# Optimization experiments

Measured on AMD Instinct MI355X. Metric: run time of the kernel, lower is better.

Reference implementation:

```python
import jax, jax.numpy as jnp
import numpy as np

N = 100000
E = 1600000
U_DIM = 8
H_DIM = 64
MLP_H = 32
LRELU_SLOPE = 0.01  # torch LeakyReLU default


def _linear_params(key, fan_in, fan_out):
    # torch nn.Linear init: U(-1/sqrt(fan_in), 1/sqrt(fan_in))
    k1, k2 = jax.random.split(key)
    bound = 1.0 / np.sqrt(fan_in)
    W = jax.random.uniform(k1, (fan_in, fan_out), minval=-bound, maxval=bound, dtype=jnp.float32)
    b = jax.random.uniform(k2, (fan_out,), minval=-bound, maxval=bound, dtype=jnp.float32)
    return W, b


def setup_inputs() -> dict:
    key = jax.random.key(0)
    ks = jax.random.split(key, 9)
    h = jax.random.normal(ks[0], (N, H_DIM), dtype=jnp.float32)
    u = jax.random.normal(ks[1], (N, U_DIM), dtype=jnp.float32)
    pos = jax.random.normal(ks[2], (N, 2), dtype=jnp.float32)
    src = jax.random.randint(ks[3], (E,), 0, N)
    dst = jax.random.randint(ks[4], (E,), 0, N)
    # edge MLP (u2h_enc): in = 4 + u_dim + h_dim
    W1e, b1e = _linear_params(ks[5], 4 + U_DIM + H_DIM, MLP_H)
    W2e, b2e = _linear_params(ks[6], MLP_H, H_DIM)
    # node MLP (h_updater): in = 2 + 2*h_dim + u_dim
    W1n, b1n = _linear_params(ks[7], 2 + 2 * H_DIM + U_DIM, MLP_H)
    W2n, b2n = _linear_params(ks[8], MLP_H, H_DIM)
    return {"h": h, "u": u, "pos": pos, "src": src, "dst": dst,
            "W1e": W1e, "b1e": b1e, "W2e": W2e, "b2e": b2e,
            "W1n": W1n, "b1n": b1n, "W2n": W2n, "b2n": b2n}


def _mlp(x, W1, b1, W2, b2):
    # Linear -> LeakyReLU -> Linear -> Tanh
    y = x @ W1 + b1
    y = jnp.where(y >= 0, y, LRELU_SLOPE * y)
    return jnp.tanh(y @ W2 + b2)


def reference(h, u, pos, src, dst, W1e, b1e, W2e, b2e, W1n, b1n, W2n, b2n):
    # gather: edge message input [E, 4+u+h]
    edge_inp = jnp.concatenate([pos[src], pos[dst], u[src], h[src]], axis=-1)
    msg = _mlp(edge_inp, W1e, b1e, W2e, b2e)  # [E, h_dim]
    # scatter-sum into destination nodes
    sum_h = jax.ops.segment_sum(msg, dst, num_segments=N)  # [N, h_dim]
    node_inp = jnp.concatenate([pos, h, sum_h, u], axis=-1)  # [N, 2+2h+u]
    return _mlp(node_inp, W1n, b1n, W2n, b2n)
```

## Files before the change

### kernel.cpp

```cpp
#include <hip/hip_runtime.h>


#define LRELU_SLOPE 0.01f
#define BUCK_SHIFT 8
#define TANH_SCALE 2.8853900817779268f

constexpr int OFF_W1ET  = 0;
constexpr int OFF_B1E   = 2432;
constexpr int OFF_B2E   = 4512;
constexpr int OFF_W1NA  = 4576;
constexpr int OFF_W1NS  = 7008;
constexpr int OFF_W2N   = 9056;
constexpr int OFF_B2N   = 11104;
constexpr int OFF_B1N   = 11168;
constexpr int OFF_W1POS = 11200;
constexpr int W_TOTAL   = 11264;

typedef __bf16 bf16x8 __attribute__((ext_vector_type(8)));
typedef float  f32x4  __attribute__((ext_vector_type(4)));

__device__ __forceinline__ float ftanh(float x) {
    float e = __builtin_amdgcn_exp2f(x * 2.8853900817779268f);
    return 1.0f - 2.0f * __builtin_amdgcn_rcpf(e + 1.0f);
}
__device__ __forceinline__ unsigned f2bf_pair(float f0, float f1) {
    unsigned u0 = __float_as_uint(f0), u1 = __float_as_uint(f1);
    unsigned r0 = (u0 + 0x7fffu + ((u0 >> 16) & 1u)) >> 16;
    unsigned r1 = (u1 + 0x7fffu + ((u1 >> 16) & 1u)) >> 16;
    return r0 | (r1 << 16);
}
__device__ __forceinline__ float bf_lo(unsigned p) { return __uint_as_float(p << 16); }
__device__ __forceinline__ float bf_hi(unsigned p) { return __uint_as_float(p & 0xffff0000u); }
__device__ __forceinline__ float bf_round(float f) {
    unsigned u = __float_as_uint(f);
    return __uint_as_float((u + 0x7fffu + ((u >> 16) & 1u)) & 0xffff0000u);
}
__device__ __forceinline__ bf16x8 pack8(float a0, float a1, float a2, float a3,
                                        float a4, float a5, float a6, float a7) {
    union { uint4 u; bf16x8 b; } c;
    c.u.x = f2bf_pair(a0, a1); c.u.y = f2bf_pair(a2, a3);
    c.u.z = f2bf_pair(a4, a5); c.u.w = f2bf_pair(a6, a7);
    return c.b;
}

__global__ void prep_weights(const float* __restrict__ W1e, const float* __restrict__ b1e,
                             const float* __restrict__ W2e, const float* __restrict__ b2e,
                             const float* __restrict__ W1n, const float* __restrict__ b1n,
                             const float* __restrict__ W2n, const float* __restrict__ b2n,
                             float* __restrict__ Wf, uint4* __restrict__ fragW2,
                             uint4* __restrict__ frag1, uint4* __restrict__ frag2,
                             int* __restrict__ gcnt, int nbuck) {
    int t = blockIdx.x * blockDim.x + threadIdx.x;
    int T = gridDim.x * blockDim.x;
    for (int idx = t; idx < nbuck; idx += T) gcnt[idx] = 0;
    for (int idx = t; idx < 2432; idx += T) {
        int i = idx / 32, j = idx % 32;
        Wf[OFF_W1ET + j * 76 + i] = W1e[idx];
    }
    for (int idx = t; idx < 32; idx += T)   Wf[OFF_B1E + idx] = b1e[idx];
    for (int idx = t; idx < 64; idx += T)   Wf[OFF_B2E + idx] = b2e[idx] * TANH_SCALE;
    for (int idx = t; idx < 2432; idx += T) {
        int j = idx / 76, i = idx % 76;
        float v = 0.f;
        if (i < 2)                 v = W1n[i * 32 + j];
        else if (i >= 4 && i < 12) v = W1n[(130 + (i - 4)) * 32 + j];
        else if (i >= 12)          v = W1n[(2 + (i - 12)) * 32 + j];
        Wf[OFF_W1NA + idx] = v;
    }
    for (int idx = t; idx < 64; idx += T)   Wf[OFF_B2N + idx] = b2n[idx];
    for (int idx = t; idx < 32; idx += T)   Wf[OFF_B1N + idx] = b1n[idx];
    for (int idx = t; idx < 32; idx += T) {
        Wf[OFF_W1POS + 2 * idx + 0] = W1e[2 * 32 + idx];
        Wf[OFF_W1POS + 2 * idx + 1] = W1e[3 * 32 + idx];
    }
    for (int idx = t; idx < 256; idx += T) {
        int tt = idx >> 6, l = idx & 63;
        int colv = l & 15, quadv = l >> 4;
        uint4 v;
        unsigned pk[4];
#pragma unroll
        for (int pr = 0; pr < 4; pr++) {
            int j0 = quadv * 8 + 2 * pr;
            float f0 = W2e[j0 * 64 + 16 * tt + colv] * TANH_SCALE;
            float f1 = W2e[(j0 + 1) * 64 + 16 * tt + colv] * TANH_SCALE;
            pk[pr] = f2bf_pair(f0, f1);
        }
        v.x = pk[0]; v.y = pk[1]; v.z = pk[2]; v.w = pk[3];
        fragW2[tt * 64 + l] = v;
    }
    for (int idx = t; idx < 512; idx += T) {
        int l = idx & 63, rest = idx >> 6;
        int hl = rest & 1, tt = (rest >> 1) & 1, kc = rest >> 2;
        int colv = l & 15, quadv = l >> 4;
        unsigned pk[4];
#pragma unroll
        for (int pr = 0; pr < 4; pr++) {
            int i0 = kc * 32 + quadv * 8 + 2 * pr;
            float f0 = W1n[(66 + i0) * 32 + tt * 16 + colv];
            float f1 = W1n[(66 + i0 + 1) * 32 + tt * 16 + colv];
            if (hl) { f0 -= bf_round(f0); f1 -= bf_round(f1); }
            pk[pr] = f2bf_pair(f0, f1);
        }
        uint4 v; v.x = pk[0]; v.y = pk[1]; v.z = pk[2]; v.w = pk[3];
        frag1[idx] = v;
    }
    for (int idx = t; idx < 512; idx += T) {
        int l = idx & 63, rest = idx >> 6;
        int hl = rest & 1, tt = rest >> 1;
        int colv = l & 15, quadv = l >> 4;
        unsigned pk[4];
#pragma unroll
        for (int pr = 0; pr < 4; pr++) {
            int j0 = quadv * 8 + 2 * pr;
            float f0 = W2n[j0 * 64 + tt * 16 + colv] * TANH_SCALE;
            float f1 = W2n[(j0 + 1) * 64 + tt * 16 + colv] * TANH_SCALE;
            if (hl) { f0 -= bf_round(f0); f1 -= bf_round(f1); }
            pk[pr] = f2bf_pair(f0, f1);
        }
        uint4 v; v.x = pk[0]; v.y = pk[1]; v.z = pk[2]; v.w = pk[3];
        frag2[idx] = v;
    }
}

__global__ __launch_bounds__(256) void k_phase1(
    const float* __restrict__ hbuf, const float* __restrict__ ubuf,
    const float* __restrict__ posbuf, const float* __restrict__ Wf,
    uint4* __restrict__ Abf, float* __restrict__ A2,
    const int* __restrict__ src, const int* __restrict__ dst,
    int* __restrict__ gcnt, unsigned* __restrict__ pairbuf,
    int E, int N, int C, int nblkA) {
    __shared__ int cnt[512], base[512];
    int tid = threadIdx.x;
    if ((int)blockIdx.x < nblkA) {
        for (int i = tid; i < 512; i += 256) cnt[i] = 0;
        __syncthreads();
        int e0 = blockIdx.x * 4096;
#pragma unroll
        for (int k = 0; k < 16; k++) {
            int e = e0 + k * 256 + tid;
            if (e < E) atomicAdd(&cnt[dst[e] >> BUCK_SHIFT], 1);
        }
        __syncthreads();
        for (int i = tid; i < 512; i += 256) {
            int c = cnt[i];
            base[i] = (c > 0) ? atomicAdd(&gcnt[i], c) : 0;
            cnt[i] = 0;
        }
        __syncthreads();
#pragma unroll
        for (int k = 0; k < 16; k++) {
            int e = e0 + k * 256 + tid;
            if (e < E) {
                int d = dst[e];
                int b = d >> BUCK_SHIFT;
                int r = base[b] + atomicAdd(&cnt[b], 1);
                if (r < C)
                    pairbuf[(size_t)b * C + r] =
                        (unsigned)src[e] | ((unsigned)(d & 255) << 20);
            }
        }
        return;
    }
    int n = (blockIdx.x - nblkA) * 256 + tid;
    if (n >= N) return;
    float x[76];
    float2 pp = ((const float2*)posbuf)[n];
    x[0] = pp.x; x[1] = pp.y; x[2] = 0.f; x[3] = 0.f;
    const float4* u4 = (const float4*)ubuf;
#pragma unroll
    for (int c = 0; c < 2; c++) {
        float4 uu = u4[(size_t)n * 2 + c];
        int b = 4 + 4 * c;
        x[b] = uu.x; x[b + 1] = uu.y; x[b + 2] = uu.z; x[b + 3] = uu.w;
    }
    const float4* h4 = (const float4*)hbuf;
#pragma unroll
    for (int c = 0; c < 16; c++) {
        float4 hh = h4[(size_t)n * 16 + c];
        int b = 12 + 4 * c;
        x[b] = hh.x; x[b + 1] = hh.y; x[b + 2] = hh.z; x[b + 3] = hh.w;
    }
    float ar[32];
#pragma unroll 1
    for (int j = 0; j < 32; j++) {
        const float* w1 = Wf + OFF_W1ET + j * 76;
        float a0 = Wf[OFF_B1E + j], a1 = 0.f, a2 = 0.f, a3 = 0.f;
#pragma unroll
        for (int i = 0; i < 76; i += 4) {
            a0 = fmaf(x[i + 0], w1[i + 0], a0);
            a1 = fmaf(x[i + 1], w1[i + 1], a1);
            a2 = fmaf(x[i + 2], w1[i + 2], a2);
            a3 = fmaf(x[i + 3], w1[i + 3], a3);
        }
        ar[j] = (a0 + a1) + (a2 + a3);
    }
#pragma unroll
    for (int c = 0; c < 4; c++) {
        uint4 v;
        v.x = f2bf_pair(ar[8 * c + 0], ar[8 * c + 1]);
        v.y = f2bf_pair(ar[8 * c + 2], ar[8 * c + 3]);
        v.z = f2bf_pair(ar[8 * c + 4], ar[8 * c + 5]);
        v.w = f2bf_pair(ar[8 * c + 6], ar[8 * c + 7]);
        Abf[(size_t)n * 4 + c] = v;
    }
#pragma unroll 1
    for (int j = 0; j < 32; j++) {
        const float* w1 = Wf + OFF_W1NA + j * 76;
        float a0 = Wf[OFF_B1N + j], a1 = 0.f, a2 = 0.f, a3 = 0.f;
#pragma unroll
        for (int i = 0; i < 76; i += 4) {
            a0 = fmaf(x[i + 0], w1[i + 0], a0);
            a1 = fmaf(x[i + 1], w1[i + 1], a1);
            a2 = fmaf(x[i + 2], w1[i + 2], a2);
            a3 = fmaf(x[i + 3], w1[i + 3], a3);
        }
        ar[j] = (a0 + a1) + (a2 + a3);
    }
#pragma unroll
    for (int c = 0; c < 8; c++) {
        float4 v; v.x = ar[4 * c]; v.y = ar[4 * c + 1];
        v.z = ar[4 * c + 2]; v.w = ar[4 * c + 3];
        ((float4*)(A2 + (size_t)n * 32))[c] = v;
    }
}

extern __shared__ unsigned pls[];
__global__ __launch_bounds__(256) void k_bucketB(
    const unsigned* __restrict__ pairbuf, const int* __restrict__ gcnt,
    int2* __restrict__ seg, int* __restrict__ ssrc, int N, int C) {
    __shared__ int deg[256], scn[256], exc[256], cur[256];
    int b = blockIdx.x, tid = threadIdx.x;
    int cntb = gcnt[b];
    cntb = (cntb < C) ? cntb : C;
    deg[tid] = 0; cur[tid] = 0;
    __syncthreads();
    size_t basep = (size_t)b * C;
    for (int i = tid; i < cntb; i += 256)
        atomicAdd(&deg[pairbuf[basep + i] >> 20], 1);
    __syncthreads();
    scn[tid] = deg[tid];
    __syncthreads();
    for (int st = 1; st < 256; st <<= 1) {
        int add = (tid >= st) ? scn[tid - st] : 0;
        __syncthreads();
        scn[tid] += add;
        __syncthreads();
    }
    int ex = scn[tid] - deg[tid];
    exc[tid] = ex;
    int n = (b << BUCK_SHIFT) + tid;
    if (n < N) {
        int lo = b * C + ex;
        seg[n] = make_int2(lo, lo + deg[tid]);
    }
    __syncthreads();
    for (int i = tid; i < cntb; i += 256) {
        unsigned p = pairbuf[basep + i];
        int l = (int)(p >> 20);
        int slot = exc[l] + atomicAdd(&cur[l], 1);
        pls[slot] = p & 0xFFFFFu;
    }
    __syncthreads();
    for (int i = tid; i < cntb; i += 256)
        ssrc[basep + i] = (int)pls[i];
}

__global__ __launch_bounds__(256) void fused_edge_gather(
    const int2* __restrict__ seg, const int* __restrict__ ssrc,
    const uint4* __restrict__ Abf, const float* __restrict__ posbuf,
    const float* __restrict__ Wf, const uint4* __restrict__ fragW2,
    float* __restrict__ sumh, int N, int npw) {
    int wid = blockIdx.x * 4 + (threadIdx.x >> 6);
    int lane = threadIdx.x & 63;
    int col = lane & 15, quad = lane >> 4;

    union { uint4 u; bf16x8 v; } cvt;
    bf16x8 bfr[4];
#pragma unroll
    for (int t = 0; t < 4; t++) {
        cvt.u = fragW2[t * 64 + lane];
        bfr[t] = cvt.v;
    }
    float c0[4];
#pragma unroll
    for (int t = 0; t < 4; t++) c0[t] = Wf[OFF_B2E + 16 * t + col];
    float wx[8], wy[8];
#pragma unroll
    for (int jj = 0; jj < 8; jj++) {
        float2 wv = ((const float2*)(Wf + OFF_W1POS))[quad * 8 + jj];
        wx[jj] = wv.x; wy[jj] = wv.y;
    }

    int n0 = wid * npw;
    int n1 = n0 + npw; n1 = (n1 < N) ? n1 : N;
#pragma unroll 1
    for (int n = n0; n < n1; n++) {
        int2 sg = seg[n];
        int lo = sg.x, hi = sg.y, deg = hi - lo;
        float2 pd = ((const float2*)posbuf)[n];
        float padd[8];
#pragma unroll
        for (int jj = 0; jj < 8; jj++)
            padd[jj] = fmaf(pd.x, wx[jj], pd.y * wy[jj]);

        float s0[4] = {0.f, 0.f, 0.f, 0.f};
        if (deg > 0) {
            int te = lo + col;
            te = (te < hi) ? te : (hi - 1);
            uint4 ar = Abf[(size_t)ssrc[te] * 4 + quad];
            int nfull = deg & ~15;
#pragma unroll 1
            for (int b = 0; b < nfull; b += 16) {
                int teN = lo + b + 16 + col;
                teN = (teN < hi) ? teN : (hi - 1);
                uint4 arN = Abf[(size_t)ssrc[teN] * 4 + quad];

                bf16x8 af;
                {
                    float v0 = bf_lo(ar.x) + padd[0], v1 = bf_hi(ar.x) + padd[1];
                    float v2 = bf_lo(ar.y) + padd[2], v3 = bf_hi(ar.y) + padd[3];
                    float v4 = bf_lo(ar.z) + padd[4], v5 = bf_hi(ar.z) + padd[5];
                    float v6 = bf_lo(ar.w) + padd[6], v7 = bf_hi(ar.w) + padd[7];
                    v0 = fmaxf(v0, LRELU_SLOPE * v0); v1 = fmaxf(v1, LRELU_SLOPE * v1);
                    v2 = fmaxf(v2, LRELU_SLOPE * v2); v3 = fmaxf(v3, LRELU_SLOPE * v3);
                    v4 = fmaxf(v4, LRELU_SLOPE * v4); v5 = fmaxf(v5, LRELU_SLOPE * v5);
                    v6 = fmaxf(v6, LRELU_SLOPE * v6); v7 = fmaxf(v7, LRELU_SLOPE * v7);
                    af[0] = (__bf16)v0; af[1] = (__bf16)v1; af[2] = (__bf16)v2; af[3] = (__bf16)v3;
                    af[4] = (__bf16)v4; af[5] = (__bf16)v5; af[6] = (__bf16)v6; af[7] = (__bf16)v7;
                }
#pragma unroll
                for (int t = 0; t < 4; t++) {
                    f32x4 acc = {c0[t], c0[t], c0[t], c0[t]};
                    acc = __builtin_amdgcn_mfma_f32_16x16x32_bf16(af, bfr[t], acc, 0, 0, 0);
                    float u0 = __builtin_amdgcn_exp2f(acc[0]);
                    float u1 = __builtin_amdgcn_exp2f(acc[1]);
                    float u2 = __builtin_amdgcn_exp2f(acc[2]);
                    float u3 = __builtin_amdgcn_exp2f(acc[3]);
                    float q01 = u0 + u1, q23 = u2 + u3;
                    float d01 = fmaf(u0, u1, q01) + 1.f;
                    float d23 = fmaf(u2, u3, q23) + 1.f;
                    s0[t] = fmaf(q01 + 2.f, __builtin_amdgcn_rcpf(d01), s0[t]);
                    s0[t] = fmaf(q23 + 2.f, __builtin_amdgcn_rcpf(d23), s0[t]);
                }
                ar = arN;
            }
            int tail = deg - nfull;
            if (tail) {
                bf16x8 af;
                {
                    float v0 = bf_lo(ar.x) + padd[0], v1 = bf_hi(ar.x) + padd[1];
                    float v2 = bf_lo(ar.y) + padd[2], v3 = bf_hi(ar.y) + padd[3];
                    float v4 = bf_lo(ar.z) + padd[4], v5 = bf_hi(ar.z) + padd[5];
                    float v6 = bf_lo(ar.w) + padd[6], v7 = bf_hi(ar.w) + padd[7];
                    v0 = fmaxf(v0, LRELU_SLOPE * v0); v1 = fmaxf(v1, LRELU_SLOPE * v1);
                    v2 = fmaxf(v2, LRELU_SLOPE * v2); v3 = fmaxf(v3, LRELU_SLOPE * v3);
                    v4 = fmaxf(v4, LRELU_SLOPE * v4); v5 = fmaxf(v5, LRELU_SLOPE * v5);
                    v6 = fmaxf(v6, LRELU_SLOPE * v6); v7 = fmaxf(v7, LRELU_SLOPE * v7);
                    af[0] = (__bf16)v0; af[1] = (__bf16)v1; af[2] = (__bf16)v2; af[3] = (__bf16)v3;
                    af[4] = (__bf16)v4; af[5] = (__bf16)v5; af[6] = (__bf16)v6; af[7] = (__bf16)v7;
                }
                int rowb = quad * 4;
#pragma unroll
                for (int t = 0; t < 4; t++) {
                    f32x4 acc = {c0[t], c0[t], c0[t], c0[t]};
                    acc = __builtin_amdgcn_mfma_f32_16x16x32_bf16(af, bfr[t], acc, 0, 0, 0);
                    float u0 = (rowb + 0 < tail) ? __builtin_amdgcn_exp2f(acc[0]) : 1e30f;
                    float u1 = (rowb + 1 < tail) ? __builtin_amdgcn_exp2f(acc[1]) : 1e30f;
                    float u2 = (rowb + 2 < tail) ? __builtin_amdgcn_exp2f(acc[2]) : 1e30f;
                    float u3 = (rowb + 3 < tail) ? __builtin_amdgcn_exp2f(acc[3]) : 1e30f;
                    float q01 = u0 + u1, q23 = u2 + u3;
                    float d01 = fmaf(u0, u1, q01) + 1.f;
                    float d23 = fmaf(u2, u3, q23) + 1.f;
                    s0[t] = fmaf(q01 + 2.f, __builtin_amdgcn_rcpf(d01), s0[t]);
                    s0[t] = fmaf(q23 + 2.f, __builtin_amdgcn_rcpf(d23), s0[t]);
                }
            }
        }
#pragma unroll
        for (int t = 0; t < 4; t++) {
            s0[t] += __shfl_xor(s0[t], 16);
            s0[t] += __shfl_xor(s0[t], 32);
        }
        if (lane < 16) {
            float* sr = sumh + (size_t)n * 64;
            float fd = (float)deg;
#pragma unroll
            for (int t = 0; t < 4; t++) sr[16 * t + lane] = fmaf(-2.f, s0[t], fd);
        }
    }
}

__global__ __launch_bounds__(256) void k_node4(
    const float* __restrict__ A2, const float* __restrict__ sumh,
    const float* __restrict__ Wf, const uint4* __restrict__ frag1,
    const uint4* __restrict__ frag2, float* __restrict__ out,
    int N, int ngroups) {
    __shared__ float ylds[4 * 16 * 36];
    int wv = threadIdx.x >> 6, lane = threadIdx.x & 63;
    int col = lane & 15, quad = lane >> 4;
    int g = blockIdx.x * 4 + wv;
    bool live = (g < ngroups);
    int gc = live ? g : (ngroups - 1);
    int nbase = gc * 16;

    int nA = nbase + col; nA = (nA < N) ? nA : (N - 1);
    const float* srow = sumh + (size_t)nA * 64 + quad * 8;
    bf16x8 sh[2], sl[2];
#pragma unroll
    for (int kc = 0; kc < 2; kc++) {
        float4 f0 = *(const float4*)(srow + kc * 32);
        float4 f1 = *(const float4*)(srow + kc * 32 + 4);
        sh[kc] = pack8(f0.x, f0.y, f0.z, f0.w, f1.x, f1.y, f1.z, f1.w);
        sl[kc] = pack8(f0.x - bf_round(f0.x), f0.y - bf_round(f0.y),
                       f0.z - bf_round(f0.z), f0.w - bf_round(f0.w),
                       f1.x - bf_round(f1.x), f1.y - bf_round(f1.y),
                       f1.z - bf_round(f1.z), f1.w - bf_round(f1.w));
    }

    f32x4 acc1[2];
#pragma unroll
    for (int t = 0; t < 2; t++) { f32x4 z = {0.f, 0.f, 0.f, 0.f}; acc1[t] = z; }
#pragma unroll
    for (int kc = 0; kc < 2; kc++) {
#pragma unroll
        for (int t = 0; t < 2; t++) {
            union { uint4 u; bf16x8 b; } bh, bl;
            bh.u = frag1[((kc * 2 + t) * 2 + 0) * 64 + lane];
            bl.u = frag1[((kc * 2 + t) * 2 + 1) * 64 + lane];
            acc1[t] = __builtin_amdgcn_mfma_f32_16x16x32_bf16(sh[kc], bh.b, acc1[t], 0, 0, 0);
            acc1[t] = __builtin_amdgcn_mfma_f32_16x16x32_bf16(sh[kc], bl.b, acc1[t], 0, 0, 0);
            acc1[t] = __builtin_amdgcn_mfma_f32_16x16x32_bf16(sl[kc], bh.b, acc1[t], 0, 0, 0);
        }
    }

    float* yw = ylds + wv * 576;
#pragma unroll
    for (int t = 0; t < 2; t++) {
#pragma unroll
        for (int r = 0; r < 4; r++) {
            int ndr = quad * 4 + r;
            int nd = nbase + ndr; nd = (nd < N) ? nd : (N - 1);
            float yv = acc1[t][r] + A2[(size_t)nd * 32 + t * 16 + col];
            yv = fmaxf(yv, LRELU_SLOPE * yv);
            yw[ndr * 36 + t * 16 + col] = yv;
        }
    }
    __syncthreads();

    const float* yr = ylds + wv * 576 + col * 36 + quad * 8;
    float4 y0 = *(const float4*)(yr);
    float4 y1 = *(const float4*)(yr + 4);
    bf16x8 yh = pack8(y0.x, y0.y, y0.z, y0.w, y1.x, y1.y, y1.z, y1.w);
    bf16x8 yl = pack8(y0.x - bf_round(y0.x), y0.y - bf_round(y0.y),
                      y0.z - bf_round(y0.z), y0.w - bf_round(y0.w),
                      y1.x - bf_round(y1.x), y1.y - bf_round(y1.y),
                      y1.z - bf_round(y1.z), y1.w - bf_round(y1.w));

    f32x4 acc2[4];
#pragma unroll
    for (int t = 0; t < 4; t++) {
        float b = Wf[OFF_B2N + t * 16 + col] * TANH_SCALE;
        f32x4 z = {b, b, b, b}; acc2[t] = z;
    }
#pragma unroll
    for (int t = 0; t < 4; t++) {
        union { uint4 u; bf16x8 b; } bh, bl;
        bh.u = frag2[(t * 2 + 0) * 64 + lane];
        bl.u = frag2[(t * 2 + 1) * 64 + lane];
        acc2[t] = __builtin_amdgcn_mfma_f32_16x16x32_bf16(yh, bh.b, acc2[t], 0, 0, 0);
        acc2[t] = __builtin_amdgcn_mfma_f32_16x16x32_bf16(yh, bl.b, acc2[t], 0, 0, 0);
        acc2[t] = __builtin_amdgcn_mfma_f32_16x16x32_bf16(yl, bh.b, acc2[t], 0, 0, 0);
    }
    if (live) {
#pragma unroll
        for (int t = 0; t < 4; t++) {
#pragma unroll
            for (int r = 0; r < 4; r++) {
                int nd = nbase + quad * 4 + r;
                if (nd < N) {
                    float e = __builtin_amdgcn_exp2f(acc2[t][r]);
                    out[(size_t)nd * 64 + t * 16 + col] =
                        1.f - 2.f * __builtin_amdgcn_rcpf(e + 1.f);
                }
            }
        }
    }
}

extern "C" void kernel_launch(void* const* d_in, const int* in_sizes, int n_in,
                              void* d_out, int out_size, void* d_ws, size_t ws_size,
                              hipStream_t stream) {
    const float* hbuf   = (const float*)d_in[0];
    const float* ubuf   = (const float*)d_in[1];
    const float* posbuf = (const float*)d_in[2];
    const int* src = (const int*)d_in[3];
    const int* dst = (const int*)d_in[4];

    int N = in_sizes[0] / 64;
    int E = in_sizes[3];
    int NBUCK = (N + 255) >> BUCK_SHIFT;
    int C = ((2 * ((E + NBUCK - 1) / NBUCK)) + 255) & ~255;
    int nblkA = (E + 4095) / 4096;

    char* p = (char*)d_ws;
    auto alloc = [&](size_t bytes) {
        char* r = p;
        p += (bytes + 255) & ~(size_t)255;
        return r;
    };
    float*    Wf      = (float*)alloc(W_TOTAL * 4);
    uint4*    fragW2  = (uint4*)alloc(4 * 64 * 16);
    uint4*    frag1   = (uint4*)alloc(512 * 16);
    uint4*    frag2   = (uint4*)alloc(512 * 16);
    uint4*    Abf     = (uint4*)alloc((size_t)N * 64);
    float*    A2      = (float*)alloc((size_t)N * 32 * 4);
    float*    sumh    = (float*)alloc((size_t)N * 64 * 4);
    int2*     seg     = (int2*)alloc((size_t)N * 8);
    int*      gcnt    = (int*)alloc((size_t)NBUCK * 4);
    unsigned* pairbuf = (unsigned*)alloc((size_t)NBUCK * C * 4);
    int*      ssrc    = (int*)alloc((size_t)NBUCK * C * 4);

    prep_weights<<<32, 256, 0, stream>>>(
        (const float*)d_in[5], (const float*)d_in[6],
        (const float*)d_in[7], (const float*)d_in[8],
        (const float*)d_in[9], (const float*)d_in[10],
        (const float*)d_in[11], (const float*)d_in[12], Wf, fragW2,
        frag1, frag2, gcnt, NBUCK);

    int nblkP = nblkA + (N + 255) / 256;
    k_phase1<<<nblkP, 256, 0, stream>>>(
        hbuf, ubuf, posbuf, Wf, Abf, A2, src, dst, gcnt, pairbuf, E, N, C, nblkA);

    k_bucketB<<<NBUCK, 256, (size_t)C * 4, stream>>>(
        pairbuf, gcnt, seg, ssrc, N, C);

    const int FBLK = 2048;
    int npw = (N + FBLK * 4 - 1) / (FBLK * 4);
    fused_edge_gather<<<FBLK, 256, 0, stream>>>(
        seg, ssrc, Abf, posbuf, Wf, fragW2, sumh, N, npw);

    int ngroups = (N + 15) / 16;
    k_node4<<<(ngroups + 3) / 4, 256, 0, stream>>>(
        A2, sumh, Wf, frag1, frag2, (float*)d_out, N, ngroups);
}
```

Before: 240.6 us.

## Compute per-node first-layer projections with split-bf16 MFMA instead of scalar FMAs

```diff
diff --git a/kernel.cpp b/kernel.cpp
--- a/kernel.cpp
+++ b/kernel.cpp
@@ -5,12 +5,8 @@
 #define BUCK_SHIFT 8
 #define TANH_SCALE 2.8853900817779268f
 
-constexpr int OFF_W1ET  = 0;
 constexpr int OFF_B1E   = 2432;
 constexpr int OFF_B2E   = 4512;
-constexpr int OFF_W1NA  = 4576;
-constexpr int OFF_W1NS  = 7008;
-constexpr int OFF_W2N   = 9056;
 constexpr int OFF_B2N   = 11104;
 constexpr int OFF_B1N   = 11168;
 constexpr int OFF_W1POS = 11200;
@@ -19,10 +15,6 @@
 typedef __bf16 bf16x8 __attribute__((ext_vector_type(8)));
 typedef float  f32x4  __attribute__((ext_vector_type(4)));
 
-__device__ __forceinline__ float ftanh(float x) {
-    float e = __builtin_amdgcn_exp2f(x * 2.8853900817779268f);
-    return 1.0f - 2.0f * __builtin_amdgcn_rcpf(e + 1.0f);
-}
 __device__ __forceinline__ unsigned f2bf_pair(float f0, float f1) {
     unsigned u0 = __float_as_uint(f0), u1 = __float_as_uint(f1);
     unsigned r0 = (u0 + 0x7fffu + ((u0 >> 16) & 1u)) >> 16;
@@ -43,30 +35,34 @@
     return c.b;
 }
 
+__device__ __forceinline__ float w1e_x96(const float* W1e, int i, int j) {
+    if (i < 64) return W1e[(12 + i) * 32 + j];
+    if (i == 64) return W1e[0 * 32 + j];
+    if (i == 65) return W1e[1 * 32 + j];
+    if (i >= 68 && i < 76) return W1e[(4 + i - 68) * 32 + j];
+    return 0.f;
+}
+__device__ __forceinline__ float w1n_x96(const float* W1n, int i, int j) {
+    if (i < 64) return W1n[(2 + i) * 32 + j];
+    if (i == 64) return W1n[0 * 32 + j];
+    if (i == 65) return W1n[1 * 32 + j];
+    if (i >= 68 && i < 76) return W1n[(130 + i - 68) * 32 + j];
+    return 0.f;
+}
+
 __global__ void prep_weights(const float* __restrict__ W1e, const float* __restrict__ b1e,
                              const float* __restrict__ W2e, const float* __restrict__ b2e,
                              const float* __restrict__ W1n, const float* __restrict__ b1n,
                              const float* __restrict__ W2n, const float* __restrict__ b2n,
                              float* __restrict__ Wf, uint4* __restrict__ fragW2,
                              uint4* __restrict__ frag1, uint4* __restrict__ frag2,
+                             uint4* __restrict__ fragE, uint4* __restrict__ fragN,
                              int* __restrict__ gcnt, int nbuck) {
     int t = blockIdx.x * blockDim.x + threadIdx.x;
     int T = gridDim.x * blockDim.x;
     for (int idx = t; idx < nbuck; idx += T) gcnt[idx] = 0;
-    for (int idx = t; idx < 2432; idx += T) {
-        int i = idx / 32, j = idx % 32;
-        Wf[OFF_W1ET + j * 76 + i] = W1e[idx];
-    }
     for (int idx = t; idx < 32; idx += T)   Wf[OFF_B1E + idx] = b1e[idx];
     for (int idx = t; idx < 64; idx += T)   Wf[OFF_B2E + idx] = b2e[idx] * TANH_SCALE;
-    for (int idx = t; idx < 2432; idx += T) {
-        int j = idx / 76, i = idx % 76;
-        float v = 0.f;
-        if (i < 2)                 v = W1n[i * 32 + j];
-        else if (i >= 4 && i < 12) v = W1n[(130 + (i - 4)) * 32 + j];
-        else if (i >= 12)          v = W1n[(2 + (i - 12)) * 32 + j];
-        Wf[OFF_W1NA + idx] = v;
-    }
     for (int idx = t; idx < 64; idx += T)   Wf[OFF_B2N + idx] = b2n[idx];
     for (int idx = t; idx < 32; idx += T)   Wf[OFF_B1N + idx] = b1n[idx];
     for (int idx = t; idx < 32; idx += T) {
@@ -120,23 +116,48 @@
         uint4 v; v.x = pk[0]; v.y = pk[1]; v.z = pk[2]; v.w = pk[3];
         frag2[idx] = v;
     }
+    for (int idx = t; idx < 768; idx += T) {
+        int l = idx & 63, rest = idx >> 6;
+        int hl = rest & 1, tt = (rest >> 1) & 1, kc = rest >> 2;
+        int colv = l & 15, quadv = l >> 4;
+        int j = tt * 16 + colv;
+        unsigned pkE[4], pkN[4];
+#pragma unroll
+        for (int pr = 0; pr < 4; pr++) {
+            int i0 = kc * 32 + quadv * 8 + 2 * pr;
+            float e0 = w1e_x96(W1e, i0, j), e1 = w1e_x96(W1e, i0 + 1, j);
+            float n0 = w1n_x96(W1n, i0, j), n1 = w1n_x96(W1n, i0 + 1, j);
+            if (hl) {
+                e0 -= bf_round(e0); e1 -= bf_round(e1);
+                n0 -= bf_round(n0); n1 -= bf_round(n1);
+            }
+            pkE[pr] = f2bf_pair(e0, e1);
+            pkN[pr] = f2bf_pair(n0, n1);
+        }
+        uint4 ve; ve.x = pkE[0]; ve.y = pkE[1]; ve.z = pkE[2]; ve.w = pkE[3];
+        uint4 vn; vn.x = pkN[0]; vn.y = pkN[1]; vn.z = pkN[2]; vn.w = pkN[3];
+        fragE[idx] = ve;
+        fragN[idx] = vn;
+    }
 }
 
 __global__ __launch_bounds__(256) void k_phase1(
     const float* __restrict__ hbuf, const float* __restrict__ ubuf,
     const float* __restrict__ posbuf, const float* __restrict__ Wf,
+    const uint4* __restrict__ fragE, const uint4* __restrict__ fragN,
     uint4* __restrict__ Abf, float* __restrict__ A2,
     const int* __restrict__ src, const int* __restrict__ dst,
     int* __restrict__ gcnt, unsigned* __restrict__ pairbuf,
     int E, int N, int C, int nblkA) {
     __shared__ int cnt[512], base[512];
+    __shared__ float tileE[4 * 16 * 36], tileN[4 * 16 * 36];
     int tid = threadIdx.x;
     if ((int)blockIdx.x < nblkA) {
         for (int i = tid; i < 512; i += 256) cnt[i] = 0;
         __syncthreads();
-        int e0 = blockIdx.x * 4096;
-#pragma unroll
-        for (int k = 0; k < 16; k++) {
+        int e0 = blockIdx.x * 2048;
+#pragma unroll
+        for (int k = 0; k < 8; k++) {
             int e = e0 + k * 256 + tid;
             if (e < E) atomicAdd(&cnt[dst[e] >> BUCK_SHIFT], 1);
         }
@@ -148,7 +169,7 @@
         }
         __syncthreads();
 #pragma unroll
-        for (int k = 0; k < 16; k++) {
+        for (int k = 0; k < 8; k++) {
             int e = e0 + k * 256 + tid;
             if (e < E) {
                 int d = dst[e];
@@ -161,107 +182,145 @@
         }
         return;
     }
-    int n = (blockIdx.x - nblkA) * 256 + tid;
-    if (n >= N) return;
-    float x[76];
-    float2 pp = ((const float2*)posbuf)[n];
-    x[0] = pp.x; x[1] = pp.y; x[2] = 0.f; x[3] = 0.f;
-    const float4* u4 = (const float4*)ubuf;
-#pragma unroll
-    for (int c = 0; c < 2; c++) {
-        float4 uu = u4[(size_t)n * 2 + c];
-        int b = 4 + 4 * c;
-        x[b] = uu.x; x[b + 1] = uu.y; x[b + 2] = uu.z; x[b + 3] = uu.w;
-    }
-    const float4* h4 = (const float4*)hbuf;
-#pragma unroll
-    for (int c = 0; c < 16; c++) {
-        float4 hh = h4[(size_t)n * 16 + c];
-        int b = 12 + 4 * c;
-        x[b] = hh.x; x[b + 1] = hh.y; x[b + 2] = hh.z; x[b + 3] = hh.w;
-    }
-    float ar[32];
-#pragma unroll 1
-    for (int j = 0; j < 32; j++) {
-        const float* w1 = Wf + OFF_W1ET + j * 76;
-        float a0 = Wf[OFF_B1E + j], a1 = 0.f, a2 = 0.f, a3 = 0.f;
-#pragma unroll
-        for (int i = 0; i < 76; i += 4) {
-            a0 = fmaf(x[i + 0], w1[i + 0], a0);
-            a1 = fmaf(x[i + 1], w1[i + 1], a1);
-            a2 = fmaf(x[i + 2], w1[i + 2], a2);
-            a3 = fmaf(x[i + 3], w1[i + 3], a3);
-        }
-        ar[j] = (a0 + a1) + (a2 + a3);
-    }
-#pragma unroll
-    for (int c = 0; c < 4; c++) {
+    int wv = tid >> 6, lane = tid & 63;
+    int col = lane & 15, quad = lane >> 4;
+    int g = ((int)blockIdx.x - nblkA) * 4 + wv;
+    int ngroups = (N + 15) >> 4;
+    if (g >= ngroups) return;
+    int nbase = g * 16;
+    int nA = nbase + col; nA = (nA < N) ? nA : (N - 1);
+
+    bf16x8 xh[3], xl[3];
+    {
+        const float* hrow = hbuf + (size_t)nA * 64 + quad * 8;
+        float4 f0 = *(const float4*)(hrow);
+        float4 f1 = *(const float4*)(hrow + 4);
+        xh[0] = pack8(f0.x, f0.y, f0.z, f0.w, f1.x, f1.y, f1.z, f1.w);
+        xl[0] = pack8(f0.x - bf_round(f0.x), f0.y - bf_round(f0.y),
+                      f0.z - bf_round(f0.z), f0.w - bf_round(f0.w),
+                      f1.x - bf_round(f1.x), f1.y - bf_round(f1.y),
+                      f1.z - bf_round(f1.z), f1.w - bf_round(f1.w));
+        float4 g0 = *(const float4*)(hrow + 32);
+        float4 g1 = *(const float4*)(hrow + 36);
+        xh[1] = pack8(g0.x, g0.y, g0.z, g0.w, g1.x, g1.y, g1.z, g1.w);
+        xl[1] = pack8(g0.x - bf_round(g0.x), g0.y - bf_round(g0.y),
+                      g0.z - bf_round(g0.z), g0.w - bf_round(g0.w),
+                      g1.x - bf_round(g1.x), g1.y - bf_round(g1.y),
+                      g1.z - bf_round(g1.z), g1.w - bf_round(g1.w));
+    }
+    {
+        float xv[8];
+#pragma unroll
+        for (int i = 0; i < 8; i++) xv[i] = 0.f;
+        if (quad == 0) {
+            float2 pp = ((const float2*)posbuf)[nA];
+            float4 uu = ((const float4*)ubuf)[(size_t)nA * 2];
+            xv[0] = pp.x; xv[1] = pp.y;
+            xv[4] = uu.x; xv[5] = uu.y; xv[6] = uu.z; xv[7] = uu.w;
+        } else if (quad == 1) {
+            float4 ub = ((const float4*)ubuf)[(size_t)nA * 2 + 1];
+            xv[0] = ub.x; xv[1] = ub.y; xv[2] = ub.z; xv[3] = ub.w;
+        }
+        xh[2] = pack8(xv[0], xv[1], xv[2], xv[3], xv[4], xv[5], xv[6], xv[7]);
+        xl[2] = pack8(xv[0] - bf_round(xv[0]), xv[1] - bf_round(xv[1]),
+                      xv[2] - bf_round(xv[2]), xv[3] - bf_round(xv[3]),
+                      xv[4] - bf_round(xv[4]), xv[5] - bf_round(xv[5]),
+                      xv[6] - bf_round(xv[6]), xv[7] - bf_round(xv[7]));
+    }
+
+    f32x4 accE[2], accN[2];
+#pragma unroll
+    for (int t = 0; t < 2; t++) {
+        float be = Wf[OFF_B1E + t * 16 + col];
+        float bn = Wf[OFF_B1N + t * 16 + col];
+        f32x4 e = {be, be, be, be}; accE[t] = e;
+        f32x4 n = {bn, bn, bn, bn}; accN[t] = n;
+    }
+#pragma unroll
+    for (int kc = 0; kc < 3; kc++) {
+#pragma unroll
+        for (int t = 0; t < 2; t++) {
+            union { uint4 u; bf16x8 b; } bh, bl;
+            int fi = ((kc * 2 + t) * 2) * 64 + lane;
+            bh.u = fragE[fi]; bl.u = fragE[fi + 64];
+            accE[t] = __builtin_amdgcn_mfma_f32_16x16x32_bf16(xh[kc], bh.b, accE[t], 0, 0, 0);
+            accE[t] = __builtin_amdgcn_mfma_f32_16x16x32_bf16(xh[kc], bl.b, accE[t], 0, 0, 0);
+            accE[t] = __builtin_amdgcn_mfma_f32_16x16x32_bf16(xl[kc], bh.b, accE[t], 0, 0, 0);
+            bh.u = fragN[fi]; bl.u = fragN[fi + 64];
+            accN[t] = __builtin_amdgcn_mfma_f32_16x16x32_bf16(xh[kc], bh.b, accN[t], 0, 0, 0);
+            accN[t] = __builtin_amdgcn_mfma_f32_16x16x32_bf16(xh[kc], bl.b, accN[t], 0, 0, 0);
+            accN[t] = __builtin_amdgcn_mfma_f32_16x16x32_bf16(xl[kc], bh.b, accN[t], 0, 0, 0);
+        }
+    }
+
+    float* twE = tileE + wv * 576;
+    float* twN = tileN + wv * 576;
+#pragma unroll
+    for (int t = 0; t < 2; t++) {
+#pragma unroll
+        for (int r = 0; r < 4; r++) {
+            twE[(quad * 4 + r) * 36 + t * 16 + col] = accE[t][r];
+            twN[(quad * 4 + r) * 36 + t * 16 + col] = accN[t][r];
+        }
+    }
+    {
+        int node = lane >> 2, q = lane & 3;
+        const float* tr = twE + node * 36 + q * 8;
         uint4 v;
-        v.x = f2bf_pair(ar[8 * c + 0], ar[8 * c + 1]);
-        v.y = f2bf_pair(ar[8 * c + 2], ar[8 * c + 3]);
-        v.z = f2bf_pair(ar[8 * c + 4], ar[8 * c + 5]);
-        v.w = f2bf_pair(ar[8 * c + 6], ar[8 * c + 7]);
-        Abf[(size_t)n * 4 + c] = v;
-    }
-#pragma unroll 1
-    for (int j = 0; j < 32; j++) {
-        const float* w1 = Wf + OFF_W1NA + j * 76;
-        float a0 = Wf[OFF_B1N + j], a1 = 0.f, a2 = 0.f, a3 = 0.f;
-#pragma unroll
-        for (int i = 0; i < 76; i += 4) {
-            a0 = fmaf(x[i + 0], w1[i + 0], a0);
-            a1 = fmaf(x[i + 1], w1[i + 1], a1);
-            a2 = fmaf(x[i + 2], w1[i + 2], a2);
-            a3 = fmaf(x[i + 3], w1[i + 3], a3);
-        }
-        ar[j] = (a0 + a1) + (a2 + a3);
-    }
-#pragma unroll
-    for (int c = 0; c < 8; c++) {
-        float4 v; v.x = ar[4 * c]; v.y = ar[4 * c + 1];
-        v.z = ar[4 * c + 2]; v.w = ar[4 * c + 3];
-        ((float4*)(A2 + (size_t)n * 32))[c] = v;
+        v.x = f2bf_pair(tr[0], tr[1]); v.y = f2bf_pair(tr[2], tr[3]);
+        v.z = f2bf_pair(tr[4], tr[5]); v.w = f2bf_pair(tr[6], tr[7]);
+        if (nbase + node < N) Abf[(size_t)(nbase + node) * 4 + q] = v;
+    }
+#pragma unroll
+    for (int it = 0; it < 2; it++) {
+        int fi = lane + it * 64;
+        int node = fi >> 3, c = fi & 7;
+        float4 fv = *(const float4*)(twN + node * 36 + c * 4);
+        if (nbase + node < N)
+            ((float4*)(A2 + (size_t)(nbase + node) * 32))[c] = fv;
     }
 }
 
 extern __shared__ unsigned pls[];
-__global__ __launch_bounds__(256) void k_bucketB(
+__global__ __launch_bounds__(512) void k_bucketB(
     const unsigned* __restrict__ pairbuf, const int* __restrict__ gcnt,
     int2* __restrict__ seg, int* __restrict__ ssrc, int N, int C) {
     __shared__ int deg[256], scn[256], exc[256], cur[256];
     int b = blockIdx.x, tid = threadIdx.x;
     int cntb = gcnt[b];
     cntb = (cntb < C) ? cntb : C;
-    deg[tid] = 0; cur[tid] = 0;
+    if (tid < 256) { deg[tid] = 0; cur[tid] = 0; }
     __syncthreads();
     size_t basep = (size_t)b * C;
-    for (int i = tid; i < cntb; i += 256)
+    for (int i = tid; i < cntb; i += 512)
         atomicAdd(&deg[pairbuf[basep + i] >> 20], 1);
     __syncthreads();
-    scn[tid] = deg[tid];
+    if (tid < 256) scn[tid] = deg[tid];
     __syncthreads();
     for (int st = 1; st < 256; st <<= 1) {
-        int add = (tid >= st) ? scn[tid - st] : 0;
+        int add = (tid < 256 && tid >= st) ? scn[tid - st] : 0;
         __syncthreads();
-        scn[tid] += add;
+        if (tid < 256) scn[tid] += add;
         __syncthreads();
     }
-    int ex = scn[tid] - deg[tid];
-    exc[tid] = ex;
-    int n = (b << BUCK_SHIFT) + tid;
-    if (n < N) {
-        int lo = b * C + ex;
-        seg[n] = make_int2(lo, lo + deg[tid]);
+    if (tid < 256) {
+        int ex = scn[tid] - deg[tid];
+        exc[tid] = ex;
+        int n = (b << BUCK_SHIFT) + tid;
+        if (n < N) {
+            int lo = b * C + ex;
+            seg[n] = make_int2(lo, lo + deg[tid]);
+        }
     }
     __syncthreads();
-    for (int i = tid; i < cntb; i += 256) {
+    for (int i = tid; i < cntb; i += 512) {
         unsigned p = pairbuf[basep + i];
         int l = (int)(p >> 20);
         int slot = exc[l] + atomicAdd(&cur[l], 1);
         pls[slot] = p & 0xFFFFFu;
     }
     __syncthreads();
-    for (int i = tid; i < cntb; i += 256)
+    for (int i = tid; i < cntb; i += 512)
         ssrc[basep + i] = (int)pls[i];
 }
 
@@ -500,7 +559,7 @@
     int E = in_sizes[3];
     int NBUCK = (N + 255) >> BUCK_SHIFT;
     int C = ((2 * ((E + NBUCK - 1) / NBUCK)) + 255) & ~255;
-    int nblkA = (E + 4095) / 4096;
+    int nblkA = (E + 2047) / 2048;
 
     char* p = (char*)d_ws;
     auto alloc = [&](size_t bytes) {
@@ -512,6 +571,8 @@
     uint4*    fragW2  = (uint4*)alloc(4 * 64 * 16);
     uint4*    frag1   = (uint4*)alloc(512 * 16);
     uint4*    frag2   = (uint4*)alloc(512 * 16);
+    uint4*    fragE   = (uint4*)alloc(768 * 16);
+    uint4*    fragN   = (uint4*)alloc(768 * 16);
     uint4*    Abf     = (uint4*)alloc((size_t)N * 64);
     float*    A2      = (float*)alloc((size_t)N * 32 * 4);
     float*    sumh    = (float*)alloc((size_t)N * 64 * 4);
@@ -525,13 +586,15 @@
         (const float*)d_in[7], (const float*)d_in[8],
         (const float*)d_in[9], (const float*)d_in[10],
         (const float*)d_in[11], (const float*)d_in[12], Wf, fragW2,
-        frag1, frag2, gcnt, NBUCK);
-
-    int nblkP = nblkA + (N + 255) / 256;
+        frag1, frag2, fragE, fragN, gcnt, NBUCK);
+
+    int ngroups = (N + 15) / 16;
+    int nblkP = nblkA + (ngroups + 3) / 4;
     k_phase1<<<nblkP, 256, 0, stream>>>(
-        hbuf, ubuf, posbuf, Wf, Abf, A2, src, dst, gcnt, pairbuf, E, N, C, nblkA);
-
-    k_bucketB<<<NBUCK, 256, (size_t)C * 4, stream>>>(
+        hbuf, ubuf, posbuf, Wf, fragE, fragN, Abf, A2, src, dst,
+        gcnt, pairbuf, E, N, C, nblkA);
+
+    k_bucketB<<<NBUCK, 512, (size_t)C * 4, stream>>>(
         pairbuf, gcnt, seg, ssrc, N, C);
 
     const int FBLK = 2048;
@@ -539,7 +602,6 @@
     fused_edge_gather<<<FBLK, 256, 0, stream>>>(
         seg, ssrc, Abf, posbuf, Wf, fragW2, sumh, N, npw);
 
-    int ngroups = (N + 15) / 16;
     k_node4<<<(ngroups + 3) / 4, 256, 0, stream>>>(
         A2, sumh, Wf, frag1, frag2, (float*)d_out, N, ngroups);
 }
```

Result: faster. 235.4 us (-2.2%).
